# Kernel optimization log

Hardware: AMD Instinct MI355X
Metric: run time of the kernel (lower is better)

The kernel has to match this reference:

```python
import jax, jax.numpy as jnp
import numpy as np
from jax import lax

# Dims from LSTMTagger class constants
B, S, LP = 1024, 128, 14       # sentences, words/sentence, padded chars/word
K, CE, WE, Lf = 3, 6, 10, 4    # char window, char emb, word emb, cnn filters
H, V, A, T = 6, 50000, 100, 135  # lstm hidden, vocab, alphabet, tagset
D = WE + Lf                     # lstm input dim = 14
LW = LP - K + 1                 # conv windows per word = 12


def setup_inputs() -> dict:
    key = jax.random.key(0)
    ks = jax.random.split(key, 14)
    n = lambda k, shp: jax.random.normal(k, shp, dtype=jnp.float32) * 0.1
    inp = {
        "word_idx": jax.random.randint(ks[0], (B, S), 0, V, dtype=jnp.int32),
        "char_idx": jax.random.randint(ks[1], (B, S, LP), 0, A, dtype=jnp.int32),
        "word_emb": n(ks[2], (V, WE)),
        "char_emb": n(ks[3], (A, CE)),
        "Wc": n(ks[4], (Lf, K * CE)),   # Conv1d(1, l, K*CE) weight, squeezed
        "bc": n(ks[5], (Lf,)),
        "Wih_f": n(ks[6], (4 * H, D)),
        "Whh_f": n(ks[7], (4 * H, H)),
        "b_f": n(ks[8], (4 * H,)),      # b_ih + b_hh fused (equivalent)
        "Wih_b": n(ks[9], (4 * H, D)),
        "Whh_b": n(ks[10], (4 * H, H)),
        "b_b": n(ks[11], (4 * H,)),
        "Wt": n(ks[12], (T, 2 * H)),
        "bt": n(ks[13], (T,)),
    }
    return inp


def _lstm_scan(xs, Wih, Whh, b):
    # xs: [S, B, D] -> hs: [S, B, H]; torch gate order i, f, g, o
    h0 = jnp.zeros((xs.shape[1], H), xs.dtype)

    def step(carry, xt):
        h, c = carry
        g = xt @ Wih.T + h @ Whh.T + b
        i, f, gg, o = jnp.split(g, 4, axis=-1)
        c = jax.nn.sigmoid(f) * c + jax.nn.sigmoid(i) * jnp.tanh(gg)
        h = jax.nn.sigmoid(o) * jnp.tanh(c)
        return (h, c), h

    _, hs = lax.scan(step, (h0, h0), xs)
    return hs


def reference(word_emb, char_emb, Wc, bc, Wih_f, Whh_f, b_f,
              Wih_b, Whh_b, b_b, Wt, bt, word_idx, char_idx):
    # per-word char CNN: sliding K-char windows, flatten, linear, max-pool
    ce = char_emb[char_idx]                              # [B,S,LP,CE]
    windows = jnp.concatenate([ce[:, :, i:i + LW] for i in range(K)], axis=-1)  # [B,S,LW,K*CE]
    phi = jnp.einsum('bswk,lk->bswl', windows, Wc) + bc  # [B,S,LW,Lf]
    char_repr = phi.max(axis=2)                          # [B,S,Lf]

    we = word_emb[word_idx]                              # [B,S,WE]
    x = jnp.concatenate([we, char_repr], axis=-1)        # [B,S,D]

    xs = x.transpose(1, 0, 2)                            # [S,B,D]
    hf = _lstm_scan(xs, Wih_f, Whh_f, b_f)               # forward direction
    hb = _lstm_scan(xs[::-1], Wih_b, Whh_b, b_b)[::-1]   # backward direction
    out = jnp.concatenate([hf, hb], axis=-1).transpose(1, 0, 2)  # [B,S,2H]

    tag_space = out @ Wt.T + bt                          # [B,S,T]
    return jax.nn.log_softmax(tag_space, axis=-1)
```

## Files before the change

### kernel.cpp

```cpp
#include <hip/hip_runtime.h>

#define B_   1024
#define S_   128
#define LP_  14
#define K_   3
#define CE_  6
#define WE_  10
#define LF_  4
#define H_   6
#define D_   14
#define T_   135
#define LW_  12
#define V_   50000
#define A_   100

static __device__ __forceinline__ float sigm(float x) {
    float e = __expf(-fabsf(x));
    float r = __frcp_rn(1.0f + e);
    return (x >= 0.f) ? r : e * r;
}
static __device__ __forceinline__ float tanh_(float x) {
    float e = __expf(-2.0f * fabsf(x));
    float r = (1.0f - e) * __frcp_rn(1.0f + e);
    return (x >= 0.f) ? r : -r;
}

__global__ __launch_bounds__(256) void k_fused(
    const int* __restrict__ word_idx, const int* __restrict__ char_idx,
    const float* __restrict__ word_emb, const float* __restrict__ char_emb,
    const float* __restrict__ Wc, const float* __restrict__ bc,
    const float* __restrict__ Wih_f, const float* __restrict__ Whh_f, const float* __restrict__ b_f,
    const float* __restrict__ Wih_b, const float* __restrict__ Whh_b, const float* __restrict__ b_b,
    const float* __restrict__ Wt, const float* __restrict__ bt,
    float* __restrict__ out)
{
    __shared__ float s_x[512][16];
    __shared__ float s_h[4][S_][12];
    __shared__ float s_ce[A_ * CE_];
    __shared__ float s_wc[LF_ * K_ * CE_];
    __shared__ float s_bc[LF_];

    int t = threadIdx.x;
    for (int e = t; e < A_ * CE_; e += 256) s_ce[e] = char_emb[e];
    if (t < LF_ * K_ * CE_) s_wc[t] = Wc[t];
    if (t < LF_) s_bc[t] = bc[t];
    __syncthreads();

    int Wbase = blockIdx.x * 512;
    #pragma unroll
    for (int rep = 0; rep < 2; ++rep) {
        int wl = t + rep * 256;
        int w  = Wbase + wl;
        const int2* ci2 = (const int2*)(char_idx + (size_t)w * LP_);
        int idxs[LP_];
        #pragma unroll
        for (int p = 0; p < 7; ++p) {
            int2 v = ci2[p];
            idxs[2 * p] = v.x; idxs[2 * p + 1] = v.y;
        }
        float ce[LP_][CE_];
        #pragma unroll
        for (int p = 0; p < LP_; ++p) {
            int idx = idxs[p];
            idx = idx < 0 ? 0 : (idx >= A_ ? A_ - 1 : idx);
            #pragma unroll
            for (int c = 0; c < CE_; ++c) ce[p][c] = s_ce[idx * CE_ + c];
        }
        float xr[16];
        #pragma unroll
        for (int l = 0; l < LF_; ++l) {
            float acc[LW_];
            float bl = s_bc[l];
            #pragma unroll
            for (int q = 0; q < LW_; ++q) acc[q] = bl;
            #pragma unroll
            for (int kk = 0; kk < K_; ++kk) {
                #pragma unroll
                for (int c = 0; c < CE_; ++c) {
                    float wv_ = s_wc[l * (K_ * CE_) + kk * CE_ + c];
                    #pragma unroll
                    for (int q = 0; q < LW_; ++q) acc[q] = fmaf(ce[q + kk][c], wv_, acc[q]);
                }
            }
            float m = acc[0];
            #pragma unroll
            for (int q = 1; q < LW_; ++q) m = fmaxf(m, acc[q]);
            xr[WE_ + l] = m;
        }
        int wi = word_idx[w];
        wi = wi < 0 ? 0 : (wi >= V_ ? V_ - 1 : wi);
        const float2* wep = (const float2*)(word_emb + (size_t)wi * WE_);
        #pragma unroll
        for (int c = 0; c < WE_ / 2; ++c) {
            float2 v = wep[c];
            xr[2 * c] = v.x; xr[2 * c + 1] = v.y;
        }
        xr[14] = 0.f; xr[15] = 0.f;
        float4* xp = (float4*)&s_x[wl][0];
        xp[0] = make_float4(xr[0], xr[1], xr[2], xr[3]);
        xp[1] = make_float4(xr[4], xr[5], xr[6], xr[7]);
        xp[2] = make_float4(xr[8], xr[9], xr[10], xr[11]);
        xp[3] = make_float4(xr[12], xr[13], xr[14], xr[15]);
    }
    __syncthreads();

    int wv   = t >> 6;
    int lane = t & 63;
    int dir  = lane >> 5;
    int l    = lane & 31;
    bool act = (l < 24);
    int u = act ? (l % 6) : 0;
    int j = act ? (l / 6) : 0;
    int base = dir << 5;
    bool isg = (j == 2);

    {
        const float* Wih = dir ? Wih_b : Wih_f;
        const float* Whh = dir ? Whh_b : Whh_f;
        const float* bi  = dir ? b_b  : b_f;
        int r = j * H_ + u;
        float wih[D_], whh[H_], bias;
        #pragma unroll
        for (int k = 0; k < D_; ++k) wih[k] = Wih[r * D_ + k];
        #pragma unroll
        for (int k = 0; k < H_; ++k) whh[k] = Whh[r * H_ + k];
        bias = bi[r];

        float h[H_];
        #pragma unroll
        for (int k = 0; k < H_; ++k) h[k] = 0.f;
        float c = 0.f;

        float ax = bias;
        {
            const float* xp = &s_x[wv * S_ + (dir ? S_ - 1 : 0)][0];
            #pragma unroll
            for (int k = 0; k < D_; ++k) ax = fmaf(wih[k], xp[k], ax);
        }
        for (int s = 0; s < S_; ++s) {
            int se = dir ? (S_ - 1 - s) : s;
            float a = ax;
            #pragma unroll
            for (int k = 0; k < H_; ++k) a = fmaf(whh[k], h[k], a);
            float xx = isg ? (a + a) : a;
            float sg = sigm(xx);
            float ac = isg ? fmaf(2.f, sg, -1.f) : sg;
            float vi = __shfl(ac, base + u,      64);
            float vf = __shfl(ac, base + u + 6,  64);
            float vg = __shfl(ac, base + u + 12, 64);
            float vo = __shfl(ac, base + u + 18, 64);
            c = fmaf(vf, c, vi * vg);
            float hu = vo * tanh_(c);
            if (act && j == 0) s_h[wv][se][dir * H_ + u] = hu;
            #pragma unroll
            for (int k = 0; k < H_; ++k) h[k] = __shfl(hu, base + k, 64);
            if (s + 1 < S_) {
                const float* xp = &s_x[wv * S_ + (dir ? S_ - 2 - s : s + 1)][0];
                float t2 = bias;
                #pragma unroll
                for (int k = 0; k < D_; ++k) t2 = fmaf(wih[k], xp[k], t2);
                ax = t2;
            }
        }
    }

    {
        bool has2 = (lane < T_ - 128);
        int t2c = has2 ? (lane + 128) : (T_ - 1);
        float wA[12], wB[12], wC[12];
        #pragma unroll
        for (int jj = 0; jj < 12; ++jj) {
            wA[jj] = Wt[lane * 12 + jj];
            wB[jj] = Wt[(lane + 64) * 12 + jj];
            wC[jj] = Wt[t2c * 12 + jj];
        }
        float bA = bt[lane], bB = bt[lane + 64], bC = bt[t2c];

        float* s_out = &s_x[wv * S_][0];
        float* gout  = out + ((size_t)(blockIdx.x * 4 + wv) * S_) * T_;

        for (int chunk = 0; chunk < 16; ++chunk) {
            #pragma unroll 4
            for (int it2 = 0; it2 < 8; ++it2) {
                int it = chunk * 8 + it2;
                const float4* h4 = (const float4*)&s_h[wv][it][0];
                float4 a0 = h4[0], a1 = h4[1], a2 = h4[2];
                float hv[12] = {a0.x, a0.y, a0.z, a0.w, a1.x, a1.y, a1.z, a1.w, a2.x, a2.y, a2.z, a2.w};
                float y0 = bA, y1 = bB, y2 = bC;
                #pragma unroll
                for (int jj = 0; jj < 12; ++jj) {
                    y0 = fmaf(hv[jj], wA[jj], y0);
                    y1 = fmaf(hv[jj], wB[jj], y1);
                    y2 = fmaf(hv[jj], wC[jj], y2);
                }
                float ss = __expf(y0) + __expf(y1) + (has2 ? __expf(y2) : 0.0f);
                #pragma unroll
                for (int mk = 1; mk < 64; mk <<= 1) ss += __shfl_xor(ss, mk, 64);
                float ls = __logf(ss);
                s_out[it2 * T_ + lane]      = y0 - ls;
                s_out[it2 * T_ + lane + 64] = y1 - ls;
                if (has2) s_out[it2 * T_ + lane + 128] = y2 - ls;
            }
            const float4* src = (const float4*)s_out;
            float4* dst = (float4*)(gout + (size_t)chunk * 8 * T_);
            #pragma unroll
            for (int r = 0; r < 4; ++r) dst[r * 64 + lane] = src[r * 64 + lane];
            if (lane < 270 - 256) dst[256 + lane] = src[256 + lane];
        }
    }
}

extern "C" void kernel_launch(void* const* d_in, const int* in_sizes, int n_in,
                              void* d_out, int out_size, void* d_ws, size_t ws_size,
                              hipStream_t stream)
{
    const int* word_idx = (const int*)d_in[0];
    const int* char_idx = (const int*)d_in[1];
    const float* word_emb = (const float*)d_in[2];
    const float* char_emb = (const float*)d_in[3];
    const float* Wc    = (const float*)d_in[4];
    const float* bc    = (const float*)d_in[5];
    const float* Wih_f = (const float*)d_in[6];
    const float* Whh_f = (const float*)d_in[7];
    const float* b_f   = (const float*)d_in[8];
    const float* Wih_b = (const float*)d_in[9];
    const float* Whh_b = (const float*)d_in[10];
    const float* b_b   = (const float*)d_in[11];
    const float* Wt    = (const float*)d_in[12];
    const float* bt    = (const float*)d_in[13];

    k_fused<<<B_ / 4, 256, 0, stream>>>(word_idx, char_idx, word_emb, char_emb, Wc, bc,
                                        Wih_f, Whh_f, b_f, Wih_b, Whh_b, b_b, Wt, bt,
                                        (float*)d_out);
}
```

Baseline: 194.0 us.

## Split fused kernel into LSTM kernel and separate tag projection/log-softmax kernel

The single fused kernel is split in two. The first runs the char CNN, embedding and BiLSTM and writes the hidden states to a workspace buffer. The second launches many blocks that each handle 64 words, computing the tag projection and log-softmax and writing output directly. This spreads the output-heavy projection over far more blocks than the original 256, at the cost of an extra global round trip for the hidden states and a second launch.

```diff
diff --git a/kernel.cpp b/kernel.cpp
--- a/kernel.cpp
+++ b/kernel.cpp
@@ -25,14 +25,13 @@
     return (x >= 0.f) ? r : -r;
 }
 
-__global__ __launch_bounds__(256) void k_fused(
+__global__ __launch_bounds__(256) void k_el(
     const int* __restrict__ word_idx, const int* __restrict__ char_idx,
     const float* __restrict__ word_emb, const float* __restrict__ char_emb,
     const float* __restrict__ Wc, const float* __restrict__ bc,
     const float* __restrict__ Wih_f, const float* __restrict__ Whh_f, const float* __restrict__ b_f,
     const float* __restrict__ Wih_b, const float* __restrict__ Whh_b, const float* __restrict__ b_b,
-    const float* __restrict__ Wt, const float* __restrict__ bt,
-    float* __restrict__ out)
+    float* __restrict__ hbuf)
 {
     __shared__ float s_x[512][16];
     __shared__ float s_h[4][S_][12];
@@ -163,50 +162,66 @@
             }
         }
     }
+    __syncthreads();
 
     {
-        bool has2 = (lane < T_ - 128);
-        int t2c = has2 ? (lane + 128) : (T_ - 1);
-        float wA[12], wB[12], wC[12];
+        float4* dst = (float4*)(hbuf + (size_t)blockIdx.x * 4 * S_ * 12);
+        const float4* src = (const float4*)&s_h[0][0][0];
+        #pragma unroll
+        for (int i = 0; i < 6; ++i) dst[t + 256 * i] = src[t + 256 * i];
+    }
+}
+
+__global__ __launch_bounds__(256) void k_p(
+    const float* __restrict__ hbuf,
+    const float* __restrict__ Wt, const float* __restrict__ bt,
+    float* __restrict__ out)
+{
+    __shared__ float s_hb[64 * 12];
+    int t = threadIdx.x;
+    int ib = blockIdx.x * 64;
+    {
+        const float4* src = (const float4*)(hbuf + (size_t)ib * 12);
+        float4* dst = (float4*)s_hb;
+        if (t < 192) dst[t] = src[t];
+    }
+    __syncthreads();
+
+    int lane = t & 63, wv = t >> 6;
+    bool has2 = (lane < T_ - 128);
+    int t2c = has2 ? (lane + 128) : (T_ - 1);
+
+    float wA[12], wB[12], wC[12];
+    #pragma unroll
+    for (int jj = 0; jj < 12; ++jj) {
+        wA[jj] = Wt[lane * 12 + jj];
+        wB[jj] = Wt[(lane + 64) * 12 + jj];
+        wC[jj] = Wt[t2c * 12 + jj];
+    }
+    float bA = bt[lane], bB = bt[lane + 64], bC = bt[t2c];
+
+    int it0 = wv * 16;
+    #pragma unroll 4
+    for (int k = 0; k < 16; ++k) {
+        int it = it0 + k;
+        const float4* h4 = (const float4*)(s_hb + it * 12);
+        float4 a0 = h4[0], a1 = h4[1], a2 = h4[2];
+        float hv[12] = {a0.x, a0.y, a0.z, a0.w, a1.x, a1.y, a1.z, a1.w, a2.x, a2.y, a2.z, a2.w};
+        float y0 = bA, y1 = bB, y2 = bC;
         #pragma unroll
         for (int jj = 0; jj < 12; ++jj) {
-            wA[jj] = Wt[lane * 12 + jj];
-            wB[jj] = Wt[(lane + 64) * 12 + jj];
-            wC[jj] = Wt[t2c * 12 + jj];
-        }
-        float bA = bt[lane], bB = bt[lane + 64], bC = bt[t2c];
-
-        float* s_out = &s_x[wv * S_][0];
-        float* gout  = out + ((size_t)(blockIdx.x * 4 + wv) * S_) * T_;
-
-        for (int chunk = 0; chunk < 16; ++chunk) {
-            #pragma unroll 4
-            for (int it2 = 0; it2 < 8; ++it2) {
-                int it = chunk * 8 + it2;
-                const float4* h4 = (const float4*)&s_h[wv][it][0];
-                float4 a0 = h4[0], a1 = h4[1], a2 = h4[2];
-                float hv[12] = {a0.x, a0.y, a0.z, a0.w, a1.x, a1.y, a1.z, a1.w, a2.x, a2.y, a2.z, a2.w};
-                float y0 = bA, y1 = bB, y2 = bC;
-                #pragma unroll
-                for (int jj = 0; jj < 12; ++jj) {
-                    y0 = fmaf(hv[jj], wA[jj], y0);
-                    y1 = fmaf(hv[jj], wB[jj], y1);
-                    y2 = fmaf(hv[jj], wC[jj], y2);
-                }
-                float ss = __expf(y0) + __expf(y1) + (has2 ? __expf(y2) : 0.0f);
-                #pragma unroll
-                for (int mk = 1; mk < 64; mk <<= 1) ss += __shfl_xor(ss, mk, 64);
-                float ls = __logf(ss);
-                s_out[it2 * T_ + lane]      = y0 - ls;
-                s_out[it2 * T_ + lane + 64] = y1 - ls;
-                if (has2) s_out[it2 * T_ + lane + 128] = y2 - ls;
-            }
-            const float4* src = (const float4*)s_out;
-            float4* dst = (float4*)(gout + (size_t)chunk * 8 * T_);
-            #pragma unroll
-            for (int r = 0; r < 4; ++r) dst[r * 64 + lane] = src[r * 64 + lane];
-            if (lane < 270 - 256) dst[256 + lane] = src[256 + lane];
-        }
+            y0 = fmaf(hv[jj], wA[jj], y0);
+            y1 = fmaf(hv[jj], wB[jj], y1);
+            y2 = fmaf(hv[jj], wC[jj], y2);
+        }
+        float ss = __expf(y0) + __expf(y1) + (has2 ? __expf(y2) : 0.0f);
+        #pragma unroll
+        for (int mk = 1; mk < 64; mk <<= 1) ss += __shfl_xor(ss, mk, 64);
+        float ls = __logf(ss);
+        float* op = out + (size_t)(ib + it) * T_;
+        op[lane]      = y0 - ls;
+        op[lane + 64] = y1 - ls;
+        if (has2) op[lane + 128] = y2 - ls;
     }
 }
 
@@ -229,7 +244,9 @@
     const float* Wt    = (const float*)d_in[12];
     const float* bt    = (const float*)d_in[13];
 
-    k_fused<<<B_ / 4, 256, 0, stream>>>(word_idx, char_idx, word_emb, char_emb, Wc, bc,
-                                        Wih_f, Whh_f, b_f, Wih_b, Whh_b, b_b, Wt, bt,
-                                        (float*)d_out);
-}
+    float* hbuf = (float*)d_ws;
+
+    k_el<<<B_ / 4, 256, 0, stream>>>(word_idx, char_idx, word_emb, char_emb, Wc, bc,
+                                     Wih_f, Whh_f, b_f, Wih_b, Whh_b, b_b, hbuf);
+    k_p<<<(B_ * S_) / 64, 256, 0, stream>>>(hbuf, Wt, bt, (float*)d_out);
+}
```

Result: faster. 164.3 us (-15.3%).
